# Kernel optimization log

Hardware: AMD Instinct MI355X
Metric: run time of the kernel (lower is better)

The kernel has to match this reference:

```python
import jax, jax.numpy as jnp
import numpy as np

N_HEADS = 8
D_HEAD = 64  # n_embd=512 / n_heads=8


def setup_inputs() -> dict:
    key = jax.random.key(0)
    ks = jax.random.split(key, 5)
    B, T, C = 2, 4096, 512
    x = jax.random.normal(ks[0], (B, T, C), dtype=jnp.float32)
    s = 1.0 / np.sqrt(C)
    Wq = jax.random.normal(ks[1], (C, C), dtype=jnp.float32) * s
    Wk = jax.random.normal(ks[2], (C, C), dtype=jnp.float32) * s
    Wv = jax.random.normal(ks[3], (C, C), dtype=jnp.float32) * s
    Wout = jax.random.normal(ks[4], (C, C), dtype=jnp.float32) * s
    return {"x": x, "Wq": Wq, "Wk": Wk, "Wv": Wv, "Wout": Wout}


def reference(x, Wq, Wk, Wv, Wout):
    # x: [B,T,C]; nn.Linear(y) = y @ W.T, here weights stored as [C,C] used directly
    B, T, C = x.shape
    H, D = N_HEADS, D_HEAD
    q = (x @ Wq.T).reshape(B, T, H, D).transpose(0, 2, 1, 3)  # [B,H,T,D]
    k = (x @ Wk.T).reshape(B, T, H, D).transpose(0, 2, 1, 3)
    v = (x @ Wv.T).reshape(B, T, H, D).transpose(0, 2, 1, 3)
    att = jnp.einsum('bhqd,bhkd->bhqk', q, k) / jnp.sqrt(jnp.float32(D))  # [B,H,T,T]
    causal = jnp.tril(jnp.ones((T, T), dtype=bool))
    att = jnp.where(causal, att, -jnp.inf)
    att = jax.nn.softmax(att, axis=-1)
    # dropout is identity in eval mode (p=0)
    y = jnp.einsum('bhqk,bhkd->bhqd', att, v)  # [B,H,T,D]
    y = y.transpose(0, 2, 1, 3).reshape(B, T, C)
    return y @ Wout.T
```

## Files before the change

kernel.cpp:

```cpp
#include <hip/hip_runtime.h>
#include <hip/hip_bf16.h>
#include <math.h>
#include <stdint.h>

using bf16 = __hip_bfloat16;
typedef __attribute__((ext_vector_type(8))) short short8;
typedef __attribute__((ext_vector_type(4))) short short4v;
typedef __attribute__((ext_vector_type(4))) float float4v;

#define MFMA16(a, b, c) __builtin_amdgcn_mfma_f32_16x16x32_bf16(a, b, c, 0, 0, 0)

__device__ __forceinline__ short bfbits(float f) {
  bf16 h = (bf16)f;
  return *(short*)&h;
}

__device__ __forceinline__ short8 ld_cvt8(const float* p) {
  union { float4v v[2]; float f[8]; } u;
  u.v[0] = *(const float4v*)p;
  u.v[1] = *(const float4v*)(p + 4);
  short8 r;
#pragma unroll
  for (int j = 0; j < 8; j++) r[j] = bfbits(u.f[j]);
  return r;
}

__device__ __forceinline__ void gload16(const bf16* g, bf16* l) {
  __builtin_amdgcn_global_load_lds(
      (const __attribute__((address_space(1))) void*)g,
      (__attribute__((address_space(3))) void*)l, 16, 0, 0);
}

__global__ __launch_bounds__(256) void conv_all(
    const float* __restrict__ x, const float* __restrict__ w0,
    const float* __restrict__ w1, const float* __restrict__ w2,
    const float* __restrict__ w3, bf16* __restrict__ cx,
    bf16* __restrict__ cw) {
  size_t gid = ((size_t)blockIdx.x * 256 + threadIdx.x) * 8;
  const float* src;
  bf16* dst;
  size_t off;
  if (gid < 4194304) {
    src = x; dst = cx; off = gid;
  } else {
    size_t r = gid - 4194304;
    int wi = (int)(r >> 18);
    src = wi == 0 ? w0 : wi == 1 ? w1 : wi == 2 ? w2 : w3;
    dst = cw + ((size_t)wi << 18);
    off = r & 262143;
  }
  *(short8*)(dst + off) = ld_cvt8(src + off);
}

template <int MODE, int MT>
__device__ __forceinline__ void gemm_body(bf16* As, bf16* Bs,
                                          const bf16* __restrict__ A,
                                          const bf16* __restrict__ W,
                                          void* __restrict__ outp,
                                          float oscale) {
  constexpr int MI = MT / 32;
  constexpr int ASZ = MT * 64;
  constexpr int BSZ = 128 * 64;
  const int bm = blockIdx.x * MT, bn = blockIdx.y * 128;
  const int tid = threadIdx.x;
  const int lane = tid & 63;
  const int wave = tid >> 6;
  const int lr = lane & 15, quad = lane >> 4;
  const int wm = (wave & 1) * (MT / 2), wn = (wave >> 1) * 64;

  const int srow = lane >> 3;
  const int scl = (lane & 7) ^ (srow & 7);
  const int rsw = lr & 7;

  float4v acc[MI][4] = {};

  auto stage = [&](int k0, int b) {
    bf16* Ad = As + b * ASZ;
    bf16* Bd = Bs + b * BSZ;
#pragma unroll
    for (int j = 0; j < MT / 32; j++) {
      const int m = wave + 4 * j;
      gload16(&A[(size_t)(bm + 8 * m + srow) * 512 + k0 + scl * 8],
              &Ad[(8 * m) * 64]);
    }
#pragma unroll
    for (int j = 0; j < 4; j++) {
      const int m = wave + 4 * j;
      gload16(&W[(size_t)(bn + 8 * m + srow) * 512 + k0 + scl * 8],
              &Bd[(8 * m) * 64]);
    }
  };

  stage(0, 0);
  __syncthreads();

  for (int s = 0; s < 8; s++) {
    if (s + 1 < 8) stage(64 * (s + 1), (s + 1) & 1);
    const bf16* Ac = As + (s & 1) * ASZ;
    const bf16* Bc = Bs + (s & 1) * BSZ;
#pragma unroll
    for (int kk = 0; kk < 2; kk++) {
      short8 af[MI], bfv[4];
#pragma unroll
      for (int i = 0; i < MI; i++)
        af[i] = *(const short8*)
            &Ac[(wm + i * 16 + lr) * 64 + ((4 * kk + quad) ^ rsw) * 8];
#pragma unroll
      for (int i = 0; i < 4; i++)
        bfv[i] = *(const short8*)
            &Bc[(wn + i * 16 + lr) * 64 + ((4 * kk + quad) ^ rsw) * 8];
#pragma unroll
      for (int mi = 0; mi < MI; mi++)
#pragma unroll
        for (int ni = 0; ni < 4; ni++)
          acc[mi][ni] = MFMA16(af[mi], bfv[ni], acc[mi][ni]);
    }
    __syncthreads();
  }

  const int row0 = bm + wm + quad * 4;
  const int col0 = bn + wn + lr;
#pragma unroll
  for (int mi = 0; mi < MI; mi++) {
#pragma unroll
    for (int ni = 0; ni < 4; ni++) {
      const int col = col0 + ni * 16;
      if (MODE == 1) {
        float* out = (float*)outp;
#pragma unroll
        for (int i = 0; i < 4; i++) {
          int m = row0 + mi * 16 + i;
          out[(size_t)m * 512 + col] = acc[mi][ni][i];
        }
      } else if (MODE == 0) {
        bf16* out = (bf16*)outp;
        const int hh = col >> 6, d = col & 63;
#pragma unroll
        for (int i = 0; i < 4; i++) {
          int m = row0 + mi * 16 + i;
          int bb = m >> 12, t = m & 4095;
          out[(((size_t)(bb * 8 + hh) * 4096 + t) << 6) + d] =
              (bf16)(acc[mi][ni][i] * oscale);
        }
      } else {
        bf16* out = (bf16*)outp;
        const int hh = col >> 6, d = col & 63;
        int m0 = row0 + mi * 16;
        int bb = m0 >> 12, t0 = m0 & 4095;
        short4v pk;
#pragma unroll
        for (int i = 0; i < 4; i++) pk[i] = bfbits(acc[mi][ni][i]);
        *(short4v*)&out[(((size_t)(bb * 8 + hh) * 64 + d) << 12) + t0] = pk;
      }
    }
  }
}

#define QSCALE 0.18033688f

__global__ __launch_bounds__(256) void qkv_kernel(
    const bf16* __restrict__ cx, const bf16* __restrict__ cW,
    bf16* q, bf16* k, bf16* vt) {
  __shared__ __align__(16) bf16 As[2 * 128 * 64];
  __shared__ __align__(16) bf16 Bs[2 * 128 * 64];
  if (blockIdx.z == 0)      gemm_body<0, 128>(As, Bs, cx, cW, q, QSCALE);
  else if (blockIdx.z == 1) gemm_body<0, 128>(As, Bs, cx, cW + 262144, k, 1.0f);
  else                      gemm_body<2, 128>(As, Bs, cx, cW + 2 * 262144, vt, 1.0f);
}

__global__ __launch_bounds__(256) void proj_kernel(
    const bf16* __restrict__ y, const bf16* __restrict__ cWout,
    float* __restrict__ out) {
  __shared__ __align__(16) bf16 As[2 * 64 * 64];
  __shared__ __align__(16) bf16 Bs[2 * 128 * 64];
  gemm_body<1, 64>(As, Bs, y, cWout, out, 1.0f);
}

__device__ __forceinline__ int lsw(int row, int col) {
  return (row << 6) + (col ^ ((row & 7) << 3));
}

template <bool DIAG>
__device__ __forceinline__ void attn_step(const bf16* __restrict__ Kc,
                                          const bf16* __restrict__ Vc,
                                          short8 qf0, short8 qf1, short8 ones,
                                          int wave, int lr, int quad,
                                          float4v& Lacc, float4v* O) {
  float4v S[4] = {};
  __builtin_amdgcn_s_setprio(1);
#pragma unroll
  for (int nc = 0; nc < 4; nc++) {
    short8 kf0 = *(const short8*)&Kc[lsw(nc * 16 + lr, quad * 8)];
    short8 kf1 = *(const short8*)&Kc[lsw(nc * 16 + lr, 32 + quad * 8)];
    S[nc] = MFMA16(kf0, qf0, S[nc]);
    S[nc] = MFMA16(kf1, qf1, S[nc]);
  }
  __builtin_amdgcn_s_setprio(0);

  short8 pf0, pf1;
#pragma unroll
  for (int nc = 0; nc < 4; nc++) {
#pragma unroll
    for (int i = 0; i < 4; i++) {
      float pv = exp2f(S[nc][i]);
      if (DIAG) {
        int kl = nc * 16 + quad * 4 + i;
        pv = (kl > wave * 16 + lr) ? 0.f : pv;
      }
      short bb = bfbits(pv);
      if (nc == 0)      pf0[i] = bb;
      else if (nc == 1) pf0[4 + i] = bb;
      else if (nc == 2) pf1[i] = bb;
      else              pf1[4 + i] = bb;
    }
  }

  __builtin_amdgcn_s_setprio(1);
  Lacc = MFMA16(pf0, ones, Lacc);
  Lacc = MFMA16(pf1, ones, Lacc);

#pragma unroll
  for (int nc = 0; nc < 4; nc++) {
    const int row = nc * 16 + lr;
    short8 vfa = *(const short8*)&Vc[lsw(row, quad * 8)];
    short8 vfb = *(const short8*)&Vc[lsw(row, 32 + quad * 8)];
    O[nc] = MFMA16(pf0, vfa, O[nc]);
    O[nc] = MFMA16(pf1, vfb, O[nc]);
  }
  __builtin_amdgcn_s_setprio(0);
}

__device__ __forceinline__ void vstore_perm(bf16* Vb, int row, int vA,
                                            short8 rv) {
  short4v lo = __builtin_shufflevector(rv, rv, 0, 1, 2, 3);
  short4v hi = __builtin_shufflevector(rv, rv, 4, 5, 6, 7);
  *(short4v*)&Vb[lsw(row, vA)] = lo;
  *(short4v*)&Vb[lsw(row, vA + 8)] = hi;
}

__global__ __launch_bounds__(512, 4) void attn_kernel(const bf16* __restrict__ Qg,
                                                      const bf16* __restrict__ Kg,
                                                      const bf16* __restrict__ Vtg,
                                                      bf16* __restrict__ Y) {
  constexpr int T = 4096;
  __shared__ __align__(16) bf16 KV[2][2][2][64 * 64];

  const int bx = blockIdx.x;
  const int p = bx >> 4;
  const int pB = 63 - p;
  const int hb = bx & 15;
  const int h = hb >> 1, b = hb & 1;
  const size_t ho = ((size_t)(b * 8 + h)) * T * 64;
  const bf16* Qh = Qg + ho;
  const bf16* Kh = Kg + ho;
  const bf16* Vth = Vtg + ho;

  const int tid = threadIdx.x;
  const int G = tid >> 8;
  const int t = tid & 255;
  const int wave = t >> 6, lane = t & 63;
  const int lr = lane & 15, quad = lane >> 4;

  const int hA = (p + 2) >> 1;
  const int hB = (65 - p) >> 1;
  const int myA = G ? (p + 1 - hA) : hA;
  const int aB = G ? hA : 0;
  const int bB = G ? hB : 0;
  const int mysteps = myA + (G ? (64 - p - hB) : hB);

  auto kt_of = [&](int s) { return (s < myA) ? (aB + s) : (bB + (s - myA)); };

  bf16* const Kb0 = KV[G][0][0];
  bf16* const Kb1 = KV[G][1][0];
  bf16* const Vb0 = KV[G][0][1];
  bf16* const Vb1 = KV[G][1][1];

  const int srowK = lane >> 3;
  const int sclK = (lane & 7) ^ (srowK & 7);

  const int sr = t >> 3;
  const int s8 = t & 7;
  const int sc = s8 * 8;
  const int vA = 32 * (s8 >> 2) + 16 * (s8 & 1) + 4 * ((s8 >> 1) & 1);
  const bf16* vsrc0 = Vth + (size_t)sr * T + sc;
  const bf16* vsrc1 = vsrc0 + (size_t)32 * T;

  const int kt0 = kt_of(0), kt1 = kt_of(1);

  short8 rvA0 = *(const short8*)(vsrc0 + (size_t)kt0 * 64);
  short8 rvA1 = *(const short8*)(vsrc1 + (size_t)kt0 * 64);
  short8 rvB0 = *(const short8*)(vsrc0 + (size_t)kt1 * 64);
  short8 rvB1 = *(const short8*)(vsrc1 + (size_t)kt1 * 64);

#pragma unroll
  for (int j = 0; j < 2; j++) {
    const int rb = wave * 16 + 8 * j;
    gload16(&Kh[(size_t)(kt0 * 64 + rb + srowK) * 64 + sclK * 8],
            &Kb0[rb * 64]);
  }

  {
    int rr = tid >> 3, c = (tid & 7) * 8;
    *(short8*)&KV[0][1][0][lsw(rr, c)] =
        *(const short8*)&Qh[(size_t)(p * 64 + rr) * 64 + c];
    *(short8*)&KV[1][1][0][lsw(rr, c)] =
        *(const short8*)&Qh[(size_t)(pB * 64 + rr) * 64 + c];
  }
  __syncthreads();
  short8 qfA0 = *(const short8*)&KV[0][1][0][lsw(wave * 16 + lr, quad * 8)];
  short8 qfA1 = *(const short8*)&KV[0][1][0][lsw(wave * 16 + lr, 32 + quad * 8)];
  short8 qfB0 = *(const short8*)&KV[1][1][0][lsw(wave * 16 + lr, quad * 8)];
  short8 qfB1 = *(const short8*)&KV[1][1][0][lsw(wave * 16 + lr, 32 + quad * 8)];
  vstore_perm(Vb0, sr, vA, rvA0);
  vstore_perm(Vb0, sr + 32, vA, rvA1);
  __syncthreads();

  short8 ones;
#pragma unroll
  for (int j = 0; j < 8; j++) ones[j] = (short)0x3F80;

  float4v OA[4] = {}, OB[4] = {};
  float4v LA = {}, LB = {};

#define ASTEP(S, VI0, VI1, VW0, VW1)                                          \
  {                                                                           \
    const int _s = (S);                                                       \
    if (_s + 1 < mysteps) {                                                   \
      const int ktn = kt_of(_s + 1);                                          \
      bf16* Kn = (_s & 1) ? Kb0 : Kb1;                                        \
      _Pragma("unroll")                                                       \
      for (int j = 0; j < 2; j++) {                                           \
        const int rb = wave * 16 + 8 * j;                                     \
        gload16(&Kh[(size_t)(ktn * 64 + rb + srowK) * 64 + sclK * 8],         \
                &Kn[rb * 64]);                                                \
      }                                                                       \
    }                                                                         \
    if (_s + 2 < mysteps) {                                                   \
      const int ktn = kt_of(_s + 2);                                          \
      VI0 = *(const short8*)(vsrc0 + (size_t)ktn * 64);                       \
      VI1 = *(const short8*)(vsrc1 + (size_t)ktn * 64);                       \
    }                                                                         \
    if (_s < mysteps) {                                                       \
      const bf16* Kc = (_s & 1) ? Kb1 : Kb0;                                  \
      const bf16* Vc = (_s & 1) ? Vb1 : Vb0;                                  \
      if (_s < myA) {                                                         \
        if (aB + _s == p)                                                     \
          attn_step<true>(Kc, Vc, qfA0, qfA1, ones, wave, lr, quad, LA, OA);  \
        else                                                                  \
          attn_step<false>(Kc, Vc, qfA0, qfA1, ones, wave, lr, quad, LA, OA); \
      } else {                                                                \
        if (bB + (_s - myA) == pB)                                            \
          attn_step<true>(Kc, Vc, qfB0, qfB1, ones, wave, lr, quad, LB, OB);  \
        else                                                                  \
          attn_step<false>(Kc, Vc, qfB0, qfB1, ones, wave, lr, quad, LB, OB); \
      }                                                                       \
    }                                                                         \
    if (_s + 1 < mysteps) {                                                   \
      bf16* Vn = (_s & 1) ? Vb0 : Vb1;                                        \
      vstore_perm(Vn, sr, vA, VW0);                                           \
      vstore_perm(Vn, sr + 32, vA, VW1);                                      \
    }                                                                         \
    __syncthreads();                                                          \
  }

  for (int s = 0; s < 32; s += 2) {
    ASTEP(s,     rvA0, rvA1, rvB0, rvB1);
    ASTEP(s + 1, rvB0, rvB1, rvA0, rvA1);
  }
  ASTEP(32, rvA0, rvA1, rvB0, rvB1);
#undef ASTEP

  float* OpA = (float*)&KV[1][0][0][0];
  float* OpB = (float*)&KV[1][1][0][0];
  float* LpA = (float*)&KV[0][0][0][0];
  float* LpB = LpA + 64;
  const int r0 = wave * 16 + quad * 4;
  if (G == 1) {
#pragma unroll
    for (int nc = 0; nc < 4; nc++)
#pragma unroll
      for (int i = 0; i < 4; i++) {
        OpA[(r0 + i) * 64 + nc * 16 + lr] = OA[nc][i];
        OpB[(r0 + i) * 64 + nc * 16 + lr] = OB[nc][i];
      }
    if (lr == 0) {
#pragma unroll
      for (int i = 0; i < 4; i++) { LpA[r0 + i] = LA[i]; LpB[r0 + i] = LB[i]; }
    }
  }
  __syncthreads();
  if (G == 0) {
    float invA[4], invB[4];
#pragma unroll
    for (int i = 0; i < 4; i++) {
      invA[i] = 1.f / (LA[i] + LpA[r0 + i]);
      invB[i] = 1.f / (LB[i] + LpB[r0 + i]);
    }
    const size_t ybA = ((size_t)b * T + p * 64 + r0) * 512 + h * 64;
    const size_t ybB = ((size_t)b * T + pB * 64 + r0) * 512 + h * 64;
#pragma unroll
    for (int nc = 0; nc < 4; nc++)
#pragma unroll
      for (int i = 0; i < 4; i++) {
        float oa = OA[nc][i] + OpA[(r0 + i) * 64 + nc * 16 + lr];
        float ob = OB[nc][i] + OpB[(r0 + i) * 64 + nc * 16 + lr];
        Y[ybA + (size_t)i * 512 + nc * 16 + lr] = (bf16)(oa * invA[i]);
        Y[ybB + (size_t)i * 512 + nc * 16 + lr] = (bf16)(ob * invB[i]);
      }
  }
}

extern "C" void kernel_launch(void* const* d_in, const int* in_sizes, int n_in,
                              void* d_out, int out_size, void* d_ws, size_t ws_size,
                              hipStream_t stream) {
  (void)out_size; (void)ws_size;
  const int NX = 8192 * 512;
  int xi = 0;
  for (int i = 0; i < n_in; i++)
    if (in_sizes[i] == NX) { xi = i; break; }
  const float* x = (const float*)d_in[xi];
  const float* wsrc[4];
  int wn = 0;
  for (int i = 0; i < n_in && wn < 4; i++)
    if (i != xi) wsrc[wn++] = (const float*)d_in[i];

  bf16* ws = (bf16*)d_ws;
  const size_t HE = (size_t)NX;
  bf16* q  = ws;
  bf16* k  = q + HE;
  bf16* yx = k + HE;
  bf16* cw = yx + HE;
  bf16* vt = (bf16*)d_out;
  float* out = (float*)d_out;

  conv_all<<<2560, 256, 0, stream>>>(x, wsrc[0], wsrc[1], wsrc[2], wsrc[3],
                                     yx, cw);
  qkv_kernel<<<dim3(64, 4, 3), 256, 0, stream>>>(yx, cw, q, k, vt);
  attn_kernel<<<512, 512, 0, stream>>>(q, k, vt, yx);
  proj_kernel<<<dim3(128, 4), 256, 0, stream>>>(yx, cw + 3 * 262144, out);
}
```

Before: 166.6 us.

## Load K tiles straight into registers and stream pre-permuted V via async LDS

The attention loop no longer stages K through shared memory. Each wave loads its K fragments directly from global memory into registers, prefetching the next tile while the current S/P phase runs. V is now written by the QKV GEMM epilogue in an already-permuted token order, so the attention kernel can copy it into LDS with direct global-to-LDS loads instead of a register round-trip and shuffle. Shared memory use roughly halves, with a small separate buffer for the row sums. In exchange, every wave now fetches the whole K tile redundantly from global or L2, and register pressure rises from holding eight K fragments.

```diff
diff --git a/kernel.cpp b/kernel.cpp
--- a/kernel.cpp
+++ b/kernel.cpp
@@ -147,10 +147,13 @@
         const int hh = col >> 6, d = col & 63;
         int m0 = row0 + mi * 16;
         int bb = m0 >> 12, t0 = m0 & 4095;
+        int u = t0 & 63;
+        int up = (u & 32) | ((u & 12) << 1) | ((u & 16) >> 2) | (u & 3);
         short4v pk;
 #pragma unroll
         for (int i = 0; i < 4; i++) pk[i] = bfbits(acc[mi][ni][i]);
-        *(short4v*)&out[(((size_t)(bb * 8 + hh) * 64 + d) << 12) + t0] = pk;
+        *(short4v*)&out[(((size_t)(bb * 8 + hh) * 64 + d) << 12) +
+                        (t0 & ~63) + up] = pk;
       }
     }
   }
@@ -180,23 +183,43 @@
   return (row << 6) + (col ^ ((row & 7) << 3));
 }
 
+__device__ __forceinline__ void kload(const bf16* __restrict__ Kh, int kt,
+                                      int lr, int quad, short8 (&kf)[4][2]) {
+#pragma unroll
+  for (int nc = 0; nc < 4; nc++) {
+    const bf16* r = Kh + (size_t)(kt * 64 + nc * 16 + lr) * 64 + quad * 8;
+    kf[nc][0] = *(const short8*)r;
+    kf[nc][1] = *(const short8*)(r + 32);
+  }
+}
+
+__device__ __forceinline__ void vload_lds(const bf16* __restrict__ Vth, int kt,
+                                          int wave, int srow, int scl,
+                                          bf16* Vb) {
+#pragma unroll
+  for (int j = 0; j < 2; j++) {
+    const int rb = wave * 16 + 8 * j;
+    gload16(&Vth[(size_t)(rb + srow) * 4096 + kt * 64 + scl * 8],
+            &Vb[rb * 64]);
+  }
+}
+
+__device__ __forceinline__ void qk_phase(const short8 (&kf)[4][2], short8 qf0,
+                                         short8 qf1, float4v (&S)[4]) {
+  __builtin_amdgcn_s_setprio(1);
+#pragma unroll
+  for (int nc = 0; nc < 4; nc++) {
+    S[nc] = MFMA16(kf[nc][0], qf0, S[nc]);
+    S[nc] = MFMA16(kf[nc][1], qf1, S[nc]);
+  }
+  __builtin_amdgcn_s_setprio(0);
+}
+
 template <bool DIAG>
-__device__ __forceinline__ void attn_step(const bf16* __restrict__ Kc,
-                                          const bf16* __restrict__ Vc,
-                                          short8 qf0, short8 qf1, short8 ones,
-                                          int wave, int lr, int quad,
-                                          float4v& Lacc, float4v* O) {
-  float4v S[4] = {};
-  __builtin_amdgcn_s_setprio(1);
-#pragma unroll
-  for (int nc = 0; nc < 4; nc++) {
-    short8 kf0 = *(const short8*)&Kc[lsw(nc * 16 + lr, quad * 8)];
-    short8 kf1 = *(const short8*)&Kc[lsw(nc * 16 + lr, 32 + quad * 8)];
-    S[nc] = MFMA16(kf0, qf0, S[nc]);
-    S[nc] = MFMA16(kf1, qf1, S[nc]);
-  }
-  __builtin_amdgcn_s_setprio(0);
-
+__device__ __forceinline__ void sp_phase(const float4v (&S)[4],
+                                         const bf16* __restrict__ Vc,
+                                         short8 ones, int wave, int lr,
+                                         int quad, float4v& Lacc, float4v* O) {
   short8 pf0, pf1;
 #pragma unroll
   for (int nc = 0; nc < 4; nc++) {
@@ -230,20 +253,13 @@
   __builtin_amdgcn_s_setprio(0);
 }
 
-__device__ __forceinline__ void vstore_perm(bf16* Vb, int row, int vA,
-                                            short8 rv) {
-  short4v lo = __builtin_shufflevector(rv, rv, 0, 1, 2, 3);
-  short4v hi = __builtin_shufflevector(rv, rv, 4, 5, 6, 7);
-  *(short4v*)&Vb[lsw(row, vA)] = lo;
-  *(short4v*)&Vb[lsw(row, vA + 8)] = hi;
-}
-
 __global__ __launch_bounds__(512, 4) void attn_kernel(const bf16* __restrict__ Qg,
                                                       const bf16* __restrict__ Kg,
                                                       const bf16* __restrict__ Vtg,
                                                       bf16* __restrict__ Y) {
   constexpr int T = 4096;
-  __shared__ __align__(16) bf16 KV[2][2][2][64 * 64];
+  __shared__ __align__(16) bf16 Vs[2][2][64 * 64];
+  __shared__ __align__(16) float Lx[2][64];
 
   const int bx = blockIdx.x;
   const int p = bx >> 4;
@@ -267,52 +283,29 @@
   const int aB = G ? hA : 0;
   const int bB = G ? hB : 0;
   const int mysteps = myA + (G ? (64 - p - hB) : hB);
-
   auto kt_of = [&](int s) { return (s < myA) ? (aB + s) : (bB + (s - myA)); };
 
-  bf16* const Kb0 = KV[G][0][0];
-  bf16* const Kb1 = KV[G][1][0];
-  bf16* const Vb0 = KV[G][0][1];
-  bf16* const Vb1 = KV[G][1][1];
-
-  const int srowK = lane >> 3;
-  const int sclK = (lane & 7) ^ (srowK & 7);
-
-  const int sr = t >> 3;
-  const int s8 = t & 7;
-  const int sc = s8 * 8;
-  const int vA = 32 * (s8 >> 2) + 16 * (s8 & 1) + 4 * ((s8 >> 1) & 1);
-  const bf16* vsrc0 = Vth + (size_t)sr * T + sc;
-  const bf16* vsrc1 = vsrc0 + (size_t)32 * T;
-
-  const int kt0 = kt_of(0), kt1 = kt_of(1);
-
-  short8 rvA0 = *(const short8*)(vsrc0 + (size_t)kt0 * 64);
-  short8 rvA1 = *(const short8*)(vsrc1 + (size_t)kt0 * 64);
-  short8 rvB0 = *(const short8*)(vsrc0 + (size_t)kt1 * 64);
-  short8 rvB1 = *(const short8*)(vsrc1 + (size_t)kt1 * 64);
-
-#pragma unroll
-  for (int j = 0; j < 2; j++) {
-    const int rb = wave * 16 + 8 * j;
-    gload16(&Kh[(size_t)(kt0 * 64 + rb + srowK) * 64 + sclK * 8],
-            &Kb0[rb * 64]);
-  }
+  const int srowV = lane >> 3;
+  const int sclV = (lane & 7) ^ (srowV & 7);
+
+  const int kt0 = kt_of(0);
+
+  short8 kf[4][2];
+  kload(Kh, kt0, lr, quad, kf);
+  vload_lds(Vth, kt0, wave, srowV, sclV, Vs[G][0]);
 
   {
     int rr = tid >> 3, c = (tid & 7) * 8;
-    *(short8*)&KV[0][1][0][lsw(rr, c)] =
+    *(short8*)&Vs[0][1][lsw(rr, c)] =
         *(const short8*)&Qh[(size_t)(p * 64 + rr) * 64 + c];
-    *(short8*)&KV[1][1][0][lsw(rr, c)] =
+    *(short8*)&Vs[1][1][lsw(rr, c)] =
         *(const short8*)&Qh[(size_t)(pB * 64 + rr) * 64 + c];
   }
   __syncthreads();
-  short8 qfA0 = *(const short8*)&KV[0][1][0][lsw(wave * 16 + lr, quad * 8)];
-  short8 qfA1 = *(const short8*)&KV[0][1][0][lsw(wave * 16 + lr, 32 + quad * 8)];
-  short8 qfB0 = *(const short8*)&KV[1][1][0][lsw(wave * 16 + lr, quad * 8)];
-  short8 qfB1 = *(const short8*)&KV[1][1][0][lsw(wave * 16 + lr, 32 + quad * 8)];
-  vstore_perm(Vb0, sr, vA, rvA0);
-  vstore_perm(Vb0, sr + 32, vA, rvA1);
+  short8 qfA0 = *(const short8*)&Vs[0][1][lsw(wave * 16 + lr, quad * 8)];
+  short8 qfA1 = *(const short8*)&Vs[0][1][lsw(wave * 16 + lr, 32 + quad * 8)];
+  short8 qfB0 = *(const short8*)&Vs[1][1][lsw(wave * 16 + lr, quad * 8)];
+  short8 qfB1 = *(const short8*)&Vs[1][1][lsw(wave * 16 + lr, 32 + quad * 8)];
   __syncthreads();
 
   short8 ones;
@@ -322,58 +315,31 @@
   float4v OA[4] = {}, OB[4] = {};
   float4v LA = {}, LB = {};
 
-#define ASTEP(S, VI0, VI1, VW0, VW1)                                          \
-  {                                                                           \
-    const int _s = (S);                                                       \
-    if (_s + 1 < mysteps) {                                                   \
-      const int ktn = kt_of(_s + 1);                                          \
-      bf16* Kn = (_s & 1) ? Kb0 : Kb1;                                        \
-      _Pragma("unroll")                                                       \
-      for (int j = 0; j < 2; j++) {                                           \
-        const int rb = wave * 16 + 8 * j;                                     \
-        gload16(&Kh[(size_t)(ktn * 64 + rb + srowK) * 64 + sclK * 8],         \
-                &Kn[rb * 64]);                                                \
-      }                                                                       \
-    }                                                                         \
-    if (_s + 2 < mysteps) {                                                   \
-      const int ktn = kt_of(_s + 2);                                          \
-      VI0 = *(const short8*)(vsrc0 + (size_t)ktn * 64);                       \
-      VI1 = *(const short8*)(vsrc1 + (size_t)ktn * 64);                       \
-    }                                                                         \
-    if (_s < mysteps) {                                                       \
-      const bf16* Kc = (_s & 1) ? Kb1 : Kb0;                                  \
-      const bf16* Vc = (_s & 1) ? Vb1 : Vb0;                                  \
-      if (_s < myA) {                                                         \
-        if (aB + _s == p)                                                     \
-          attn_step<true>(Kc, Vc, qfA0, qfA1, ones, wave, lr, quad, LA, OA);  \
-        else                                                                  \
-          attn_step<false>(Kc, Vc, qfA0, qfA1, ones, wave, lr, quad, LA, OA); \
-      } else {                                                                \
-        if (bB + (_s - myA) == pB)                                            \
-          attn_step<true>(Kc, Vc, qfB0, qfB1, ones, wave, lr, quad, LB, OB);  \
-        else                                                                  \
-          attn_step<false>(Kc, Vc, qfB0, qfB1, ones, wave, lr, quad, LB, OB); \
-      }                                                                       \
-    }                                                                         \
-    if (_s + 1 < mysteps) {                                                   \
-      bf16* Vn = (_s & 1) ? Vb0 : Vb1;                                        \
-      vstore_perm(Vn, sr, vA, VW0);                                           \
-      vstore_perm(Vn, sr + 32, vA, VW1);                                      \
-    }                                                                         \
-    __syncthreads();                                                          \
-  }
-
-  for (int s = 0; s < 32; s += 2) {
-    ASTEP(s,     rvA0, rvA1, rvB0, rvB1);
-    ASTEP(s + 1, rvB0, rvB1, rvA0, rvA1);
-  }
-  ASTEP(32, rvA0, rvA1, rvB0, rvB1);
-#undef ASTEP
-
-  float* OpA = (float*)&KV[1][0][0][0];
-  float* OpB = (float*)&KV[1][1][0][0];
-  float* LpA = (float*)&KV[0][0][0][0];
-  float* LpB = LpA + 64;
+  for (int s = 0; s < 33; s++) {
+    if (s + 1 < mysteps)
+      vload_lds(Vth, kt_of(s + 1), wave, srowV, sclV, Vs[G][(s + 1) & 1]);
+    if (s < mysteps) {
+      const bool isA = s < myA;
+      float4v S[4] = {};
+      qk_phase(kf, isA ? qfA0 : qfB0, isA ? qfA1 : qfB1, S);
+      if (s + 1 < mysteps) kload(Kh, kt_of(s + 1), lr, quad, kf);
+      const bf16* Vc = Vs[G][s & 1];
+      const int kt = kt_of(s);
+      if (isA) {
+        if (kt == p) sp_phase<true>(S, Vc, ones, wave, lr, quad, LA, OA);
+        else         sp_phase<false>(S, Vc, ones, wave, lr, quad, LA, OA);
+      } else {
+        if (kt == pB) sp_phase<true>(S, Vc, ones, wave, lr, quad, LB, OB);
+        else          sp_phase<false>(S, Vc, ones, wave, lr, quad, LB, OB);
+      }
+    }
+    __syncthreads();
+  }
+
+  float* OpA = (float*)&Vs[0][0][0];
+  float* OpB = (float*)&Vs[1][0][0];
+  float* LpA = Lx[0];
+  float* LpB = Lx[1];
   const int r0 = wave * 16 + quad * 4;
   if (G == 1) {
 #pragma unroll
```

After: 254.4 us. +52.7%, slower.
